# Kernel optimization log

Hardware: AMD Instinct MI355X
Metric: run time of the kernel (lower is better)

## Reference

```python
import jax, jax.numpy as jnp
import numpy as np

NH = 8
D_MODEL = 512
D_K = D_MODEL // NH
B, S = 2, 4096


def setup_inputs() -> dict:
    key = jax.random.key(0)
    ks = jax.random.split(key, 8)
    scale = 1.0 / np.sqrt(D_MODEL)
    return {
        "query": jax.random.normal(ks[0], (B, S, D_MODEL), dtype=jnp.float32),
        "key": jax.random.normal(ks[1], (B, S, D_MODEL), dtype=jnp.float32),
        "value": jax.random.normal(ks[2], (B, S, D_MODEL), dtype=jnp.float32),
        "mask": jax.random.randint(ks[3], (B, 1, S, S), 0, 2) > 0,
        "Wq": jax.random.normal(ks[4], (D_MODEL, D_MODEL), dtype=jnp.float32) * scale,
        "Wk": jax.random.normal(ks[5], (D_MODEL, D_MODEL), dtype=jnp.float32) * scale,
        "Wv": jax.random.normal(ks[6], (D_MODEL, D_MODEL), dtype=jnp.float32) * scale,
        "Wo": jax.random.normal(ks[7], (D_MODEL, D_MODEL), dtype=jnp.float32) * scale,
    }


def reference(query, key, value, mask, Wq, Wk, Wv, Wo):
    # Linear (no bias): torch Linear stores W as [out, in], y = x @ W^T.
    def proj(x, W):
        # [B, S, D] -> [B, nh, S, d_k]
        y = jnp.einsum("bsd,ed->bse", x, W)
        return y.reshape(B, S, NH, D_K).transpose(0, 2, 1, 3)

    q = proj(query, Wq)
    k = proj(key, Wk)
    v = proj(value, Wv)

    scores = jnp.einsum("bhqd,bhkd->bhqk", q, k) / jnp.sqrt(jnp.float32(D_K))
    scores = jnp.where(mask, jnp.float32(-1e9), scores)
    p_attn = jax.nn.softmax(scores, axis=-1)
    x = jnp.einsum("bhqk,bhkd->bhqd", p_attn, v)  # [B, nh, S, d_k]
    x = x.transpose(0, 2, 1, 3).reshape(B, S, D_MODEL)
    return jnp.einsum("bsd,ed->bse", x, Wo)
```

## Files before the change

### kernel.cpp

```cpp
#include <hip/hip_runtime.h>


#define S_LEN   4096
#define DM      512
#define NHEAD   8
#define DKH     64
#define NT      (S_LEN / 64)
#define LOG2E   1.44269504088896f
#define NEG2    (-1.44269504e9f)
#define MINIT   (-3.402823466e38f)
#define QSCALE  (0.125f * LOG2E)

typedef __bf16 bf16x8 __attribute__((ext_vector_type(8)));
typedef __bf16 bf16x4 __attribute__((ext_vector_type(4)));
typedef float  f32x4  __attribute__((ext_vector_type(4)));
typedef unsigned long long u64;

#define F3(a,b,c) fmaxf(fmaxf((a),(b)),(c))

__device__ inline float exp2fast(float x) {
    float r;
    asm("v_exp_f32 %0, %1" : "=v"(r) : "v"(x));
    return r;
}
__device__ inline unsigned cvtpk(float lo, float hi) {
    unsigned r;
    asm("v_cvt_pk_bf16_f32 %0, %1, %2" : "=v"(r) : "v"(lo), "v"(hi));
    return r;
}

__device__ inline void gload_lds16(const void* g, void* l) {
    __builtin_amdgcn_global_load_lds(
        (const __attribute__((address_space(1))) unsigned int*)g,
        (__attribute__((address_space(3))) unsigned int*)l, 16, 0, 0);
}

__device__ inline uint4 cvt8(float4 a, float4 b) {
    uint4 u;
    u.x = cvtpk(a.x, a.y); u.y = cvtpk(a.z, a.w);
    u.z = cvtpk(b.x, b.y); u.w = cvtpk(b.z, b.w);
    return u;
}

__global__ __launch_bounds__(256)
void prep(const int* __restrict__ mask,
          const float* __restrict__ Wq, const float* __restrict__ Wk,
          const float* __restrict__ Wv, const float* __restrict__ Wo,
          __bf16* __restrict__ wb, u64* __restrict__ bits)
{
    __shared__ u64 sm[4][64];
    const int blk = blockIdx.x, tid = threadIdx.x;

    if (blk < 512) {
        const int t = blk * 256 + tid;
        const int e = t * 8, z = e >> 18, i = e & 262143;
        const float* W = (z == 0) ? Wq : (z == 1) ? Wk : (z == 2) ? Wv : Wo;
        const float4 a = *(const float4*)&W[i];
        const float4 b = *(const float4*)&W[i + 4];
        *(uint4*)&wb[e] = cvt8(a, b);
    } else {
        const int w4 = tid >> 6, lane = tid & 63;
        const int gw = (blk - 512) * 4 + w4;
        const int p  = gw >> 6;
        const int r0 = (gw & 63) << 6;
        const int bb = p >> 6, wc = p & 63;
        #pragma unroll 4
        for (int it = 0; it < 64; ++it) {
            const int r = r0 + it;
            const size_t idx = (((size_t)(bb * S_LEN + r)) << 12) + (wc << 6) + lane;
            const u64 bal = __ballot(mask[idx] != 0);
            if (lane == 0) sm[w4][it] = bal;
        }
        bits[((size_t)p << 12) + r0 + lane] = sm[w4][lane];
    }
}

template<int MODE>
__global__ __launch_bounds__(512, 4)
void gemm_mfma(const float* __restrict__ X0, const float* __restrict__ X1,
               const float* __restrict__ X2, const __bf16* __restrict__ Xb,
               const __bf16* __restrict__ Wb,
               __bf16* __restrict__ Y0, __bf16* __restrict__ Y1,
               __bf16* __restrict__ Y2, float* __restrict__ Yf)
{
    __shared__ __align__(16) char lds[65536];

    const int tid  = threadIdx.x;
    const int lane = tid & 63;
    const int l15  = lane & 15;
    const int lhi  = lane >> 4;
    const int w    = tid >> 6;
    const int wr   = w >> 2;
    const int wc   = w & 3;
    const int row0 = blockIdx.x << 7;
    const int col0 = blockIdx.y << 7;
    const int z    = blockIdx.z;

    const float*  Xf = (z == 0) ? X0 : (z == 1) ? X1 : X2;
    const __bf16* W  = Wb + (size_t)(MODE == 0 ? z : 3) * DM * DM;

    const int sr = tid >> 2;
    const int sc = (tid & 3) << 1;

    f32x4 acc[4][2];
    #pragma unroll
    for (int m = 0; m < 4; ++m)
        #pragma unroll
        for (int n = 0; n < 2; ++n)
            acc[m][n] = (f32x4){0.f, 0.f, 0.f, 0.f};

    auto wstage = [&](int c, int k0) {
        char* Xs = lds + c * 32768;
        char* Ws = Xs + 16384;
        #pragma unroll
        for (int s = 0; s < 2; ++s) {
            const int f = w * 128 + s * 64 + lane;
            const int r = f >> 3, sl = f & 7;
            const size_t go = (size_t)r * DM + k0 + ((sl ^ (r & 7)) << 3);
            if (MODE == 1)
                gload_lds16(&Xb[(size_t)row0 * DM + go], Xs + w * 2048 + s * 1024);
            gload_lds16(&W[(size_t)col0 * DM + go], Ws + w * 2048 + s * 1024);
        }
    };

    float4 xr0, xr1, xr2, xr3;
    auto xload = [&](int k0) {
        const size_t base = (size_t)(row0 + sr) * DM + k0 + sc * 8;
        xr0 = *(const float4*)&Xf[base];
        xr1 = *(const float4*)&Xf[base + 4];
        xr2 = *(const float4*)&Xf[base + 8];
        xr3 = *(const float4*)&Xf[base + 12];
    };
    auto xwrite = [&](int c) {
        char* Xs = lds + c * 32768;
        *(uint4*)(Xs + sr * 128 + ((sc       ^ (sr & 7)) << 4)) = cvt8(xr0, xr1);
        *(uint4*)(Xs + sr * 128 + (((sc + 1) ^ (sr & 7)) << 4)) = cvt8(xr2, xr3);
    };

    wstage(0, 0);
    if (MODE == 0) { xload(0); xwrite(0); }
    __syncthreads();

    for (int t = 0; t < 8; ++t) {
        const int c = t & 1;
        if (t < 7) {
            wstage(c ^ 1, (t + 1) * 64);
            if (MODE == 0) xload((t + 1) * 64);
        }

        const char* Xs = lds + c * 32768;
        const char* Ws = Xs + 16384;
        #pragma unroll
        for (int kk = 0; kk < 2; ++kk) {
            bf16x8 xf[4], wf[2];
            #pragma unroll
            for (int m = 0; m < 4; ++m) {
                const int r = wr * 64 + m * 16 + l15;
                xf[m] = *(const bf16x8*)(Xs + r * 128 + ((((kk << 2) + lhi) ^ (r & 7)) << 4));
            }
            #pragma unroll
            for (int n = 0; n < 2; ++n) {
                const int r = wc * 32 + n * 16 + l15;
                wf[n] = *(const bf16x8*)(Ws + r * 128 + ((((kk << 2) + lhi) ^ (r & 7)) << 4));
            }
            __builtin_amdgcn_s_setprio(1);
            #pragma unroll
            for (int m = 0; m < 4; ++m)
                #pragma unroll
                for (int n = 0; n < 2; ++n)
                    acc[m][n] = __builtin_amdgcn_mfma_f32_16x16x32_bf16(wf[n], xf[m], acc[m][n], 0, 0, 0);
            __builtin_amdgcn_s_setprio(0);
        }
        if (MODE == 0 && t < 7) xwrite(c ^ 1);
        __syncthreads();
    }

    const float osc = (MODE == 0 && z == 0) ? QSCALE : 1.0f;
    #pragma unroll
    for (int m = 0; m < 4; ++m) {
        const int r = row0 + wr * 64 + m * 16 + l15;
        #pragma unroll
        for (int n = 0; n < 2; ++n) {
            const int cb = col0 + wc * 32 + n * 16 + lhi * 4;
            if (MODE == 0) {
                bf16x4 o4;
                o4[0] = (__bf16)(acc[m][n][0] * osc);
                o4[1] = (__bf16)(acc[m][n][1] * osc);
                o4[2] = (__bf16)(acc[m][n][2] * osc);
                o4[3] = (__bf16)(acc[m][n][3] * osc);
                const int bb = r >> 12, srow = r & 4095;
                const int hh = cb >> 6, dk = cb & 63;
                __bf16* Yb = (z == 0) ? Y0 : (z == 1) ? Y1 : Y2;
                *(bf16x4*)&Yb[(((size_t)(bb * NHEAD + hh)) * S_LEN + srow) * DKH + dk] = o4;
            } else {
                *(float4*)&Yf[(size_t)r * DM + cb] = *(float4*)&acc[m][n];
            }
        }
    }
}

__global__ __launch_bounds__(256, 4)
void attn_mfma(const __bf16* __restrict__ Q, const __bf16* __restrict__ K,
               const __bf16* __restrict__ V, const u64* __restrict__ bits,
               __bf16* __restrict__ ctx)
{
    __shared__ __align__(16) char lds[40960];

    const int tid  = threadIdx.x;
    const int lane = tid & 63;
    const int w    = tid >> 6;
    const int l15  = lane & 15;
    const int lhi  = lane >> 4;
    const int q0   = blockIdx.x << 6;
    const int h    = blockIdx.y;
    const int b    = blockIdx.z;

    const __bf16* Qb = Q + (size_t)(b * NHEAD + h) * S_LEN * DKH;
    const __bf16* Kb = K + (size_t)(b * NHEAD + h) * S_LEN * DKH;
    const __bf16* Vb = V + (size_t)(b * NHEAD + h) * S_LEN * DKH;

    const int qrow = q0 + w * 16 + l15;
    const u64* Mb = bits + ((size_t)b << 18) + qrow;

    const bf16x8 qa0 = *(const bf16x8*)&Qb[(size_t)qrow * DKH + lhi * 8];
    const bf16x8 qa1 = *(const bf16x8*)&Qb[(size_t)qrow * DKH + 32 + lhi * 8];

    char* psb = lds + 32768 + w * 2048;

    f32x4 o[4];
    float m_r = MINIT, l_r = 0.f;
    #pragma unroll
    for (int dt = 0; dt < 4; ++dt) o[dt] = (f32x4){0.f, 0.f, 0.f, 0.f};

    const int kr0 = tid >> 3, ks0 = tid & 7;
    const int kr1 = kr0 + 32, ks1 = ks0;
    const int vj = tid & 63, vd0 = (tid >> 6) * 8;

    auto kstage = [&](int c, int j0) {
        gload_lds16(&Kb[(size_t)(j0 + kr0) * DKH + ((ks0 ^ (kr0 & 7)) << 3)],
                    lds + c * 16384 + w * 1024);
        gload_lds16(&Kb[(size_t)(j0 + kr1) * DKH + ((ks1 ^ (kr1 & 7)) << 3)],
                    lds + c * 16384 + 4096 + w * 1024);
    };
    auto vwrite = [&](int c, uint4 va, uint4 vb2) {
        char* Vt = lds + c * 16384 + 8192;
        const __bf16* ra = (const __bf16*)&va;
        const __bf16* rb = (const __bf16*)&vb2;
        #pragma unroll
        for (int i = 0; i < 8; ++i) {
            const int d1 = vd0 + i, d2 = vd0 + 32 + i;
            *(__bf16*)(Vt + ((d1 * 128 + vj * 2) ^ ((d1 & 7) << 4))) = ra[i];
            *(__bf16*)(Vt + ((d2 * 128 + vj * 2) ^ ((d2 & 7) << 4))) = rb[i];
        }
    };

    kstage(0, 0);
    vwrite(0, *(const uint4*)&Vb[(size_t)vj * DKH + vd0],
              *(const uint4*)&Vb[(size_t)vj * DKH + vd0 + 32]);
    u64 mcur = Mb[0];
    __syncthreads();

    for (int t = 0; t < NT; ++t) {
        const int c  = t & 1;
        const int tn = (t + 1 < NT) ? (t + 1) : t;

        kstage(c ^ 1, tn << 6);
        const uint4 vna = *(const uint4*)&Vb[(size_t)((tn << 6) + vj) * DKH + vd0];
        const uint4 vnb = *(const uint4*)&Vb[(size_t)((tn << 6) + vj) * DKH + vd0 + 32];
        const u64   mnxt = Mb[(size_t)tn << 12];

        const char* Ksb = lds + c * 16384;
        const char* Vtb = Ksb + 8192;

        f32x4 s[4];
        __builtin_amdgcn_s_setprio(1);
        #pragma unroll
        for (int tt = 0; tt < 4; ++tt) {
            const int kr  = tt * 16 + l15;
            const int off = kr * 128 + ((lhi ^ (kr & 7)) << 4);
            const bf16x8 kb0 = *(const bf16x8*)(Ksb + off);
            const bf16x8 kb1 = *(const bf16x8*)(Ksb + (off ^ 64));
            f32x4 zz = (f32x4){0.f, 0.f, 0.f, 0.f};
            zz    = __builtin_amdgcn_mfma_f32_16x16x32_bf16(kb0, qa0, zz, 0, 0, 0);
            s[tt] = __builtin_amdgcn_mfma_f32_16x16x32_bf16(kb1, qa1, zz, 0, 0, 0);
        }
        __builtin_amdgcn_s_setprio(0);

        const unsigned int lo = (unsigned int)mcur, hi = (unsigned int)(mcur >> 32);
        unsigned int shf[4];
        shf[0] = lo >> (lhi << 2);
        shf[1] = lo >> (16 + (lhi << 2));
        shf[2] = hi >> (lhi << 2);
        shf[3] = hi >> (16 + (lhi << 2));

        float pv[4][4];
        #pragma unroll
        for (int tt = 0; tt < 4; ++tt)
            #pragma unroll
            for (int r = 0; r < 4; ++r)
                pv[tt][r] = ((shf[tt] >> r) & 1) ? NEG2 : s[tt][r];

        float a0 = F3(pv[0][0], pv[0][1], pv[0][2]);
        float a1 = F3(pv[0][3], pv[1][0], pv[1][1]);
        float a2 = F3(pv[1][2], pv[1][3], pv[2][0]);
        float a3 = F3(pv[2][1], pv[2][2], pv[2][3]);
        float a4 = F3(pv[3][0], pv[3][1], pv[3][2]);
        float tmax = fmaxf(F3(a0, a1, a2), F3(a3, a4, pv[3][3]));
        tmax = fmaxf(tmax, __shfl_xor(tmax, 16));
        tmax = fmaxf(tmax, __shfl_xor(tmax, 32));

        if (!__all(tmax <= m_r + 8.f)) {
            const float newm  = fmaxf(m_r, tmax);
            const float alpha = exp2fast(m_r - newm);
            m_r = newm;
            l_r *= alpha;
            #pragma unroll
            for (int dt = 0; dt < 4; ++dt) {
                o[dt][0] *= alpha; o[dt][1] *= alpha;
                o[dt][2] *= alpha; o[dt][3] *= alpha;
            }
        }

        float rsum = 0.f;
        #pragma unroll
        for (int tt = 0; tt < 4; ++tt)
            #pragma unroll
            for (int r = 0; r < 4; ++r) {
                pv[tt][r] = exp2fast(pv[tt][r] - m_r);
                rsum += pv[tt][r];
            }
        rsum += __shfl_xor(rsum, 16);
        rsum += __shfl_xor(rsum, 32);
        l_r += rsum;

        #pragma unroll
        for (int tt = 0; tt < 4; ++tt) {
            uint2 pk;
            pk.x = cvtpk(pv[tt][0], pv[tt][1]);
            pk.y = cvtpk(pv[tt][2], pv[tt][3]);
            const int off = l15 * 128
                          + ((((tt << 1) + (lhi >> 1)) ^ (l15 & 7)) << 4)
                          + ((lhi & 1) << 3);
            *(uint2*)(psb + off) = pk;
        }
        const int poff = l15 * 128 + ((lhi ^ (l15 & 7)) << 4);
        const bf16x8 pb0 = *(const bf16x8*)(psb + poff);
        const bf16x8 pb1 = *(const bf16x8*)(psb + (poff ^ 64));

        __builtin_amdgcn_s_setprio(1);
        #pragma unroll
        for (int dt = 0; dt < 4; ++dt) {
            const int vrow = dt * 16 + l15;
            const int voff = vrow * 128 + ((lhi ^ (vrow & 7)) << 4);
            const bf16x8 vb0 = *(const bf16x8*)(Vtb + voff);
            const bf16x8 vb1 = *(const bf16x8*)(Vtb + (voff ^ 64));
            o[dt] = __builtin_amdgcn_mfma_f32_16x16x32_bf16(vb0, pb0, o[dt], 0, 0, 0);
            o[dt] = __builtin_amdgcn_mfma_f32_16x16x32_bf16(vb1, pb1, o[dt], 0, 0, 0);
        }
        __builtin_amdgcn_s_setprio(0);

        vwrite(c ^ 1, vna, vnb);
        __syncthreads();
        mcur = mnxt;
    }

    const float inv = 1.f / l_r;
    #pragma unroll
    for (int dt = 0; dt < 4; ++dt) {
        bf16x4 ov;
        ov[0] = (__bf16)(o[dt][0] * inv);
        ov[1] = (__bf16)(o[dt][1] * inv);
        ov[2] = (__bf16)(o[dt][2] * inv);
        ov[3] = (__bf16)(o[dt][3] * inv);
        *(bf16x4*)&ctx[((size_t)b * S_LEN + qrow) * DM + h * DKH + dt * 16 + lhi * 4] = ov;
    }
}

extern "C" void kernel_launch(void* const* d_in, const int* in_sizes, int n_in,
                              void* d_out, int out_size, void* d_ws, size_t ws_size,
                              hipStream_t stream)
{
    const float* q    = (const float*)d_in[0];
    const float* k    = (const float*)d_in[1];
    const float* v    = (const float*)d_in[2];
    const int*   mask = (const int*)d_in[3];
    const float* Wq   = (const float*)d_in[4];
    const float* Wk   = (const float*)d_in[5];
    const float* Wv   = (const float*)d_in[6];
    const float* Wo   = (const float*)d_in[7];
    float* out = (float*)d_out;

    const size_t per = (size_t)2 * S_LEN * DM;
    __bf16* wb   = (__bf16*)d_ws;
    __bf16* Qh   = wb + (size_t)4 * DM * DM;
    __bf16* Kh   = Qh + per;
    __bf16* Vh   = Kh + per;
    __bf16* ctx  = Vh + per;
    u64*    bits = (u64*)(ctx + per);

    prep<<<dim3(2560), dim3(256), 0, stream>>>(mask, Wq, Wk, Wv, Wo, wb, bits);

    gemm_mfma<0><<<dim3(64, 4, 3), dim3(512), 0, stream>>>(
        q, k, v, nullptr, wb, Qh, Kh, Vh, nullptr);

    attn_mfma<<<dim3(64, 8, 2), dim3(256), 0, stream>>>(Qh, Kh, Vh, bits, ctx);

    gemm_mfma<1><<<dim3(64, 4, 1), dim3(512), 0, stream>>>(
        nullptr, nullptr, nullptr, ctx, wb, nullptr, nullptr, nullptr, out);
}
```

Baseline: 422.2 us.

## Store V transposed from projection GEMM and stage it with async LDS loads

The V projection epilogue now writes V in a head-major transposed [d_k, S] layout. The attention kernel can then stage V tiles into LDS with direct global-to-LDS loads instead of register loads followed by scalar transposing LDS writes. The attention block grows to 512 threads covering 128 query rows, so each K/V tile is shared by twice as many waves. The P scratch switches from an XOR swizzle to a padded stride of 144 bytes. The cost is strided scalar 2-byte global stores in the V GEMM epilogue, plus higher LDS use per block, which may reduce occupancy.

```diff
diff --git a/kernel.cpp b/kernel.cpp
--- a/kernel.cpp
+++ b/kernel.cpp
@@ -183,15 +183,22 @@
         for (int n = 0; n < 2; ++n) {
             const int cb = col0 + wc * 32 + n * 16 + lhi * 4;
             if (MODE == 0) {
-                bf16x4 o4;
-                o4[0] = (__bf16)(acc[m][n][0] * osc);
-                o4[1] = (__bf16)(acc[m][n][1] * osc);
-                o4[2] = (__bf16)(acc[m][n][2] * osc);
-                o4[3] = (__bf16)(acc[m][n][3] * osc);
                 const int bb = r >> 12, srow = r & 4095;
                 const int hh = cb >> 6, dk = cb & 63;
-                __bf16* Yb = (z == 0) ? Y0 : (z == 1) ? Y1 : Y2;
-                *(bf16x4*)&Yb[(((size_t)(bb * NHEAD + hh)) * S_LEN + srow) * DKH + dk] = o4;
+                if (z == 2) {
+                    #pragma unroll
+                    for (int i = 0; i < 4; ++i)
+                        Y2[(((size_t)(bb * NHEAD + hh)) * DKH + dk + i) * S_LEN + srow] =
+                            (__bf16)acc[m][n][i];
+                } else {
+                    bf16x4 o4;
+                    o4[0] = (__bf16)(acc[m][n][0] * osc);
+                    o4[1] = (__bf16)(acc[m][n][1] * osc);
+                    o4[2] = (__bf16)(acc[m][n][2] * osc);
+                    o4[3] = (__bf16)(acc[m][n][3] * osc);
+                    __bf16* Yb = (z == 0) ? Y0 : Y1;
+                    *(bf16x4*)&Yb[(((size_t)(bb * NHEAD + hh)) * S_LEN + srow) * DKH + dk] = o4;
+                }
             } else {
                 *(float4*)&Yf[(size_t)r * DM + cb] = *(float4*)&acc[m][n];
             }
@@ -199,25 +206,25 @@
     }
 }
 
-__global__ __launch_bounds__(256, 4)
+__global__ __launch_bounds__(512, 4)
 void attn_mfma(const __bf16* __restrict__ Q, const __bf16* __restrict__ K,
-               const __bf16* __restrict__ V, const u64* __restrict__ bits,
+               const __bf16* __restrict__ VT, const u64* __restrict__ bits,
                __bf16* __restrict__ ctx)
 {
-    __shared__ __align__(16) char lds[40960];
+    __shared__ __align__(16) char lds[51200];
 
     const int tid  = threadIdx.x;
     const int lane = tid & 63;
     const int w    = tid >> 6;
     const int l15  = lane & 15;
     const int lhi  = lane >> 4;
-    const int q0   = blockIdx.x << 6;
+    const int q0   = blockIdx.x << 7;
     const int h    = blockIdx.y;
     const int b    = blockIdx.z;
 
-    const __bf16* Qb = Q + (size_t)(b * NHEAD + h) * S_LEN * DKH;
-    const __bf16* Kb = K + (size_t)(b * NHEAD + h) * S_LEN * DKH;
-    const __bf16* Vb = V + (size_t)(b * NHEAD + h) * S_LEN * DKH;
+    const __bf16* Qb  = Q  + (size_t)(b * NHEAD + h) * S_LEN * DKH;
+    const __bf16* Kb  = K  + (size_t)(b * NHEAD + h) * S_LEN * DKH;
+    const __bf16* VbT = VT + (size_t)(b * NHEAD + h) * DKH * S_LEN;
 
     const int qrow = q0 + w * 16 + l15;
     const u64* Mb = bits + ((size_t)b << 18) + qrow;
@@ -225,38 +232,27 @@
     const bf16x8 qa0 = *(const bf16x8*)&Qb[(size_t)qrow * DKH + lhi * 8];
     const bf16x8 qa1 = *(const bf16x8*)&Qb[(size_t)qrow * DKH + 32 + lhi * 8];
 
-    char* psb = lds + 32768 + w * 2048;
+    char* psb = lds + 32768 + w * 2304;
 
     f32x4 o[4];
     float m_r = MINIT, l_r = 0.f;
     #pragma unroll
     for (int dt = 0; dt < 4; ++dt) o[dt] = (f32x4){0.f, 0.f, 0.f, 0.f};
 
-    const int kr0 = tid >> 3, ks0 = tid & 7;
-    const int kr1 = kr0 + 32, ks1 = ks0;
-    const int vj = tid & 63, vd0 = (tid >> 6) * 8;
+    const int krow = tid >> 3, kslot = tid & 7;
+    const int vrow_ = krow, vslot = kslot;
 
     auto kstage = [&](int c, int j0) {
-        gload_lds16(&Kb[(size_t)(j0 + kr0) * DKH + ((ks0 ^ (kr0 & 7)) << 3)],
+        gload_lds16(&Kb[(size_t)(j0 + krow) * DKH + ((kslot ^ (krow & 7)) << 3)],
                     lds + c * 16384 + w * 1024);
-        gload_lds16(&Kb[(size_t)(j0 + kr1) * DKH + ((ks1 ^ (kr1 & 7)) << 3)],
-                    lds + c * 16384 + 4096 + w * 1024);
     };
-    auto vwrite = [&](int c, uint4 va, uint4 vb2) {
-        char* Vt = lds + c * 16384 + 8192;
-        const __bf16* ra = (const __bf16*)&va;
-        const __bf16* rb = (const __bf16*)&vb2;
-        #pragma unroll
-        for (int i = 0; i < 8; ++i) {
-            const int d1 = vd0 + i, d2 = vd0 + 32 + i;
-            *(__bf16*)(Vt + ((d1 * 128 + vj * 2) ^ ((d1 & 7) << 4))) = ra[i];
-            *(__bf16*)(Vt + ((d2 * 128 + vj * 2) ^ ((d2 & 7) << 4))) = rb[i];
-        }
+    auto vstage = [&](int c, int j0) {
+        gload_lds16(&VbT[(size_t)vrow_ * S_LEN + j0 + ((vslot ^ (vrow_ & 7)) << 3)],
+                    lds + c * 16384 + 8192 + w * 1024);
     };
 
     kstage(0, 0);
-    vwrite(0, *(const uint4*)&Vb[(size_t)vj * DKH + vd0],
-              *(const uint4*)&Vb[(size_t)vj * DKH + vd0 + 32]);
+    vstage(0, 0);
     u64 mcur = Mb[0];
     __syncthreads();
 
@@ -265,9 +261,8 @@
         const int tn = (t + 1 < NT) ? (t + 1) : t;
 
         kstage(c ^ 1, tn << 6);
-        const uint4 vna = *(const uint4*)&Vb[(size_t)((tn << 6) + vj) * DKH + vd0];
-        const uint4 vnb = *(const uint4*)&Vb[(size_t)((tn << 6) + vj) * DKH + vd0 + 32];
-        const u64   mnxt = Mb[(size_t)tn << 12];
+        vstage(c ^ 1, tn << 6);
+        const u64 mnxt = Mb[(size_t)tn << 12];
 
         const char* Ksb = lds + c * 16384;
         const char* Vtb = Ksb + 8192;
@@ -338,20 +333,19 @@
             uint2 pk;
             pk.x = cvtpk(pv[tt][0], pv[tt][1]);
             pk.y = cvtpk(pv[tt][2], pv[tt][3]);
-            const int off = l15 * 128
-                          + ((((tt << 1) + (lhi >> 1)) ^ (l15 & 7)) << 4)
+            const int off = l15 * 144 + (((tt << 1) + (lhi >> 1)) << 4)
                           + ((lhi & 1) << 3);
             *(uint2*)(psb + off) = pk;
         }
-        const int poff = l15 * 128 + ((lhi ^ (l15 & 7)) << 4);
+        const int poff = l15 * 144 + (lhi << 4);
         const bf16x8 pb0 = *(const bf16x8*)(psb + poff);
-        const bf16x8 pb1 = *(const bf16x8*)(psb + (poff ^ 64));
+        const bf16x8 pb1 = *(const bf16x8*)(psb + poff + 64);
 
         __builtin_amdgcn_s_setprio(1);
         #pragma unroll
         for (int dt = 0; dt < 4; ++dt) {
-            const int vrow = dt * 16 + l15;
-            const int voff = vrow * 128 + ((lhi ^ (vrow & 7)) << 4);
+            const int vr  = dt * 16 + l15;
+            const int voff = vr * 128 + ((lhi ^ (vr & 7)) << 4);
             const bf16x8 vb0 = *(const bf16x8*)(Vtb + voff);
             const bf16x8 vb1 = *(const bf16x8*)(Vtb + (voff ^ 64));
             o[dt] = __builtin_amdgcn_mfma_f32_16x16x32_bf16(vb0, pb0, o[dt], 0, 0, 0);
@@ -359,7 +353,6 @@
         }
         __builtin_amdgcn_s_setprio(0);
 
-        vwrite(c ^ 1, vna, vnb);
         __syncthreads();
         mcur = mnxt;
     }
@@ -394,16 +387,16 @@
     __bf16* wb   = (__bf16*)d_ws;
     __bf16* Qh   = wb + (size_t)4 * DM * DM;
     __bf16* Kh   = Qh + per;
-    __bf16* Vh   = Kh + per;
-    __bf16* ctx  = Vh + per;
+    __bf16* VhT  = Kh + per;
+    __bf16* ctx  = VhT + per;
     u64*    bits = (u64*)(ctx + per);
 
     prep<<<dim3(2560), dim3(256), 0, stream>>>(mask, Wq, Wk, Wv, Wo, wb, bits);
 
     gemm_mfma<0><<<dim3(64, 4, 3), dim3(512), 0, stream>>>(
-        q, k, v, nullptr, wb, Qh, Kh, Vh, nullptr);
-
-    attn_mfma<<<dim3(64, 8, 2), dim3(256), 0, stream>>>(Qh, Kh, Vh, bits, ctx);
+        q, k, v, nullptr, wb, Qh, Kh, VhT, nullptr);
+
+    attn_mfma<<<dim3(32, 8, 2), dim3(512), 0, stream>>>(Qh, Kh, VhT, bits, ctx);
 
     gemm_mfma<1><<<dim3(64, 4, 1), dim3(512), 0, stream>>>(
         nullptr, nullptr, nullptr, ctx, wb, nullptr, nullptr, nullptr, out);
```

After: 394.6 us. 1.07x faster.
